# Performance work log

Measured on AMD Instinct MI355X. Metric: run time of the kernel, lower is better.

Reference implementation:

```python
import jax, jax.numpy as jnp
import numpy as np

D = 768
N_HEADS = 12
HEAD_DIM = 64
INNER = N_HEADS * HEAD_DIM
SCALE = HEAD_DIM ** -0.5
EPS = 1e-5


def setup_inputs() -> dict:
    key = jax.random.key(0)
    ks = jax.random.split(key, 7)
    s = 0.02
    return {
        "x": jax.random.normal(ks[0], (2, 2048, D), dtype=jnp.float32),
        "Wq": jax.random.normal(ks[1], (D, INNER), dtype=jnp.float32) * s,
        "Wk": jax.random.normal(ks[2], (D, INNER), dtype=jnp.float32) * s,
        "Wv": jax.random.normal(ks[3], (D, INNER), dtype=jnp.float32) * s,
        "Wo": jax.random.normal(ks[4], (INNER, D), dtype=jnp.float32) * s,
        "bo": jnp.zeros((D,), dtype=jnp.float32),
        "gamma": jnp.ones((D,), dtype=jnp.float32),
        "beta": jnp.zeros((D,), dtype=jnp.float32),
    }


def _layernorm(x, gamma, beta):
    mu = jnp.mean(x, axis=-1, keepdims=True)
    var = jnp.var(x, axis=-1, keepdims=True)
    return (x - mu) * jax.lax.rsqrt(var + EPS) * gamma + beta


def reference(x, Wq, Wk, Wv, Wo, bo, gamma, beta):
    b, n, _ = x.shape
    h = _layernorm(x, gamma, beta)
    # project and split heads: [b, n, inner] -> [b, h, n, d]
    def split(t):
        return t.reshape(b, n, N_HEADS, HEAD_DIM).transpose(0, 2, 1, 3)
    Q = split(h @ Wq)
    K = split(h @ Wk)
    V = split(h @ Wv)
    # NOTE: module applies softmax first, THEN multiplies probs by scale
    attn = jnp.einsum('bhid,bhjd->bhij', Q, K)
    attn = jax.nn.softmax(attn, axis=-1) * SCALE
    vals = jnp.einsum('bhij,bhjd->bhid', attn, V)
    vals = vals.transpose(0, 2, 1, 3).reshape(b, n, INNER)
    out = vals @ Wo + bo
    return x + out
```

## Files before the change

kernel.cpp:

```cpp
#include <hip/hip_runtime.h>
#include <stdint.h>

typedef __bf16 bf16;
typedef __bf16 bf16x8 __attribute__((ext_vector_type(8)));
typedef float  f32x4  __attribute__((ext_vector_type(4)));
typedef unsigned short u16x4 __attribute__((ext_vector_type(4)));
typedef unsigned int   u32x4v __attribute__((ext_vector_type(4)));

#define SEQ   2048
#define DM    768
#define NH    12
#define HD    64
#define ATT_SCALE 0.125f
#define LOG2E 1.44269504f
#define LN_EPS 1e-5f

__device__ __forceinline__ void gload16(const void* g, void* l) {
  __builtin_amdgcn_global_load_lds((const __attribute__((address_space(1))) void*)g,
                                   (__attribute__((address_space(3))) void*)l,
                                   16, 0, 0);
}

__global__ __launch_bounds__(256) void transpose_w(
    const float* __restrict__ Wq, const float* __restrict__ Wk,
    const float* __restrict__ Wv, const float* __restrict__ Wo,
    bf16* __restrict__ Wqkvt, bf16* __restrict__ Wot)
{
  __shared__ float tile[32][33];
  int z = blockIdx.z;
  const float* src = (z==0)?Wq:(z==1)?Wk:(z==2)?Wv:Wo;
  int r0 = blockIdx.y*32, c0 = blockIdx.x*32;
  int tx = threadIdx.x, ty = threadIdx.y;
  #pragma unroll
  for (int i=ty;i<32;i+=8) tile[i][tx] = src[(size_t)(r0+i)*DM + c0+tx];
  __syncthreads();
  bf16* dst = (z<3) ? (Wqkvt + (size_t)z*DM*DM) : Wot;
  #pragma unroll
  for (int i=ty;i<32;i+=8) dst[(size_t)(c0+i)*DM + r0+tx] = (bf16)tile[tx][i];
}

__global__ __launch_bounds__(256) void ln_kernel(
    const float* __restrict__ x, const float* __restrict__ gamma,
    const float* __restrict__ beta, bf16* __restrict__ h)
{
  int row = blockIdx.x;
  const float* xr = x + (size_t)row*DM;
  int t = threadIdx.x;
  float v0 = xr[t], v1 = xr[t+256], v2 = xr[t+512];
  float s = v0+v1+v2;
  float q = v0*v0+v1*v1+v2*v2;
  #pragma unroll
  for (int m=32;m>=1;m>>=1){ s += __shfl_xor(s,m,64); q += __shfl_xor(q,m,64); }
  __shared__ float rs[4], rq[4];
  int w = t>>6;
  if ((t&63)==0){ rs[w]=s; rq[w]=q; }
  __syncthreads();
  float S = rs[0]+rs[1]+rs[2]+rs[3];
  float Q = rq[0]+rq[1]+rq[2]+rq[3];
  float mean = S*(1.0f/DM);
  float var  = Q*(1.0f/DM) - mean*mean;
  float rstd = rsqrtf(var + LN_EPS);
  bf16* hr = h + (size_t)row*DM;
  hr[t]     = (bf16)((v0-mean)*rstd*gamma[t]     + beta[t]);
  hr[t+256] = (bf16)((v1-mean)*rstd*gamma[t+256] + beta[t+256]);
  hr[t+512] = (bf16)((v2-mean)*rstd*gamma[t+512] + beta[t+512]);
}

template<int BM, int BN, int WM, int WN, int EPI>
__global__ __launch_bounds__(256) void gemm_bt(
    const bf16* __restrict__ A, const bf16* __restrict__ Bt, int K,
    bf16* __restrict__ qk, bf16* __restrict__ vt,
    float* __restrict__ out, const float* __restrict__ bo, const float* __restrict__ xres)
{
  constexpr int MF = BM/(WM*16);
  constexpr int NF = BN/(WN*16);
  __shared__ bf16 As[BM][64];
  __shared__ bf16 Bs[BN][64];
  int tid = threadIdx.x, w = tid>>6, la = tid&63;
  int bn = blockIdx.x, bm = blockIdx.y;
  int wm = w / WN, wn = w % WN;
  int g = la>>4, li = la&15;
  int lr = la>>3, lc = (la&7)*8;
  f32x4 acc[MF][NF] = {};

  for (int kt=0; kt<K/64; ++kt) {
    int k0 = kt*64;
    #pragma unroll
    for (int i=0;i<BM/32;i++){ int c=i*4+w;
      gload16(A + ((size_t)(bm*BM + c*8 + lr))*K + k0 + lc, &As[c*8][0]); }
    #pragma unroll
    for (int i=0;i<BN/32;i++){ int c=i*4+w;
      gload16(Bt + ((size_t)(bn*BN + c*8 + lr))*K + k0 + lc, &Bs[c*8][0]); }
    __syncthreads();
    #pragma unroll
    for (int kk=0;kk<2;kk++){
      bf16x8 af[MF], bfr[NF];
      #pragma unroll
      for (int i=0;i<MF;i++) af[i]  = *(const bf16x8*)&As[wm*(BM/WM)+i*16+li][kk*32+g*8];
      #pragma unroll
      for (int j=0;j<NF;j++) bfr[j] = *(const bf16x8*)&Bs[wn*(BN/WN)+j*16+li][kk*32+g*8];
      #pragma unroll
      for (int i=0;i<MF;i++)
        #pragma unroll
        for (int j=0;j<NF;j++)
          acc[i][j] = __builtin_amdgcn_mfma_f32_16x16x32_bf16(af[i], bfr[j], acc[i][j], 0,0,0);
    }
    __syncthreads();
  }

  #pragma unroll
  for (int i=0;i<MF;i++){
    int row0 = bm*BM + wm*(BM/WM) + i*16 + g*4;
    #pragma unroll
    for (int j=0;j<NF;j++){
      int col = bn*BN + wn*(BN/WN) + j*16 + li;
      if (EPI==0){
        if (col < 1536) {
          float qs = (col < 768) ? LOG2E : 1.0f;
          #pragma unroll
          for (int r=0;r<4;r++) qk[(size_t)(row0+r)*1536 + col] = (bf16)(acc[i][j][r]*qs);
        } else {
          int cv = col - 1536; int hh = cv>>6, dd = cv&63;
          int b_ = row0>>11,  n0 = row0&2047;
          u16x4 u;
          #pragma unroll
          for (int r=0;r<4;r++){ bf16 bv = (bf16)acc[i][j][r];
            u[r] = __builtin_bit_cast(unsigned short, bv); }
          *reinterpret_cast<u16x4*>(vt + ((size_t)((b_*NH+hh)*HD+dd))*SEQ + n0) = u;
        }
      } else {
        float bb = bo[col];
        #pragma unroll
        for (int r=0;r<4;r++){ size_t idx = (size_t)(row0+r)*DM + col;
          out[idx] = acc[i][j][r] + bb + xres[idx]; }
      }
    }
  }
}

__global__ __launch_bounds__(256) void attn_kernel(
    const bf16* __restrict__ QK, const bf16* __restrict__ Vt, bf16* __restrict__ vals)
{
  __shared__ bf16 Ks[2][64][64];
  __shared__ bf16 Vs[2][64][64];
  int tid=threadIdx.x, w=tid>>6, la=tid&63;
  int qt=blockIdx.x, hh=blockIdx.y, b=blockIdx.z;
  int g=la>>4, li=la&15;
  int lr=la>>3;
  int lx=li&7;
  int lcs=((la&7)^lr)*8;
  size_t qrow0=(size_t)b*SEQ + qt*64;

  bf16x8 qf[2];
  {
    const bf16* qp = QK + (qrow0 + w*16 + li)*1536 + hh*64;
    qf[0] = *(const bf16x8*)(qp + g*8);
    qf[1] = *(const bf16x8*)(qp + 32 + g*8);
  }

  const bf16* Kbase = QK + (size_t)b*SEQ*1536 + 768 + hh*64;
  const bf16* Vbase = Vt + (size_t)(b*NH+hh)*HD*SEQ;
  #pragma unroll
  for (int i=0;i<2;i++){ int c=i*4+w;
    gload16(Kbase + (size_t)(c*8+lr)*1536 + lcs, &Ks[0][c*8][0]);
    gload16(Vbase + (size_t)(c*8+lr)*SEQ  + lcs, &Vs[0][c*8][0]); }
  __syncthreads();

  f32x4 o[4] = {};
  float lp[4] = {0.f,0.f,0.f,0.f};

  for (int t=0;t<32;t++){
    int buf=t&1;
    if (t) __syncthreads();
    if (t+1<32){
      int j0=(t+1)*64;
      #pragma unroll
      for (int i=0;i<2;i++){ int c=i*4+w;
        gload16(Kbase + (size_t)(j0+c*8+lr)*1536 + lcs, &Ks[buf^1][c*8][0]);
        gload16(Vbase + (size_t)(c*8+lr)*SEQ + j0 + lcs, &Vs[buf^1][c*8][0]); }
    }
    f32x4 s[4] = {};
    #pragma unroll
    for (int kk=0;kk<2;kk++){
      bf16x8 kf[4];
      #pragma unroll
      for (int nf=0;nf<4;nf++){
        int row = nf*16+li;
        kf[nf] = *(const bf16x8*)((const char*)&Ks[buf][0][0] + row*128 + (((kk*4+g)^lx)<<4));
      }
      __builtin_amdgcn_s_setprio(1);
      #pragma unroll
      for (int nf=0;nf<4;nf++)
        s[nf] = __builtin_amdgcn_mfma_f32_16x16x32_bf16(kf[nf], qf[kk], s[nf], 0,0,0);
      __builtin_amdgcn_s_setprio(0);
    }
    float p[4][4];
    #pragma unroll
    for (int nf=0;nf<4;nf++){
      #pragma unroll
      for (int r=0;r<4;r++){
        p[nf][r] = __builtin_amdgcn_exp2f(s[nf][r]);
        lp[nf] += p[nf][r];
      }
    }
    bf16x8 pa[2];
    #pragma unroll
    for (int ks=0;ks<2;ks++){
      unsigned int c00,c01,c10,c11;
      asm("v_cvt_pk_bf16_f32 %0, %1, %2" : "=v"(c00) : "v"(p[2*ks  ][0]), "v"(p[2*ks  ][1]));
      asm("v_cvt_pk_bf16_f32 %0, %1, %2" : "=v"(c01) : "v"(p[2*ks  ][2]), "v"(p[2*ks  ][3]));
      asm("v_cvt_pk_bf16_f32 %0, %1, %2" : "=v"(c10) : "v"(p[2*ks+1][0]), "v"(p[2*ks+1][1]));
      asm("v_cvt_pk_bf16_f32 %0, %1, %2" : "=v"(c11) : "v"(p[2*ks+1][2]), "v"(p[2*ks+1][3]));
      asm("v_permlane32_swap_b32 %0, %1" : "+v"(c00), "+v"(c10));
      asm("v_permlane32_swap_b32 %0, %1" : "+v"(c01), "+v"(c11));
      asm("v_permlane16_swap_b32 %0, %1" : "+v"(c00), "+v"(c10));
      asm("v_permlane16_swap_b32 %0, %1" : "+v"(c01), "+v"(c11));
      u32x4v cc = {c00, c01, c10, c11};
      pa[ks] = __builtin_bit_cast(bf16x8, cc);
    }
    #pragma unroll
    for (int ks=0;ks<2;ks++){
      bf16x8 vb[4];
      #pragma unroll
      for (int df=0;df<4;df++){
        int row = df*16+li;
        vb[df] = *(const bf16x8*)((const char*)&Vs[buf][0][0] + row*128 + (((ks*4+g)^lx)<<4));
      }
      __builtin_amdgcn_s_setprio(1);
      #pragma unroll
      for (int df=0;df<4;df++)
        o[df] = __builtin_amdgcn_mfma_f32_16x16x32_bf16(vb[df], pa[ks], o[df], 0,0,0);
      __builtin_amdgcn_s_setprio(0);
    }
  }
  float lsum = lp[0]+lp[1]+lp[2]+lp[3];
  lsum += __shfl_xor(lsum, 16, 64);
  lsum += __shfl_xor(lsum, 32, 64);
  float fac = ATT_SCALE / lsum;
  bf16* vrow = vals + (qrow0 + w*16 + li)*DM + hh*64;
  #pragma unroll
  for (int df=0;df<4;df++){
    u16x4 u;
    #pragma unroll
    for (int r=0;r<4;r++){
      bf16 bv = (bf16)(o[df][r] * fac);
      u[r] = __builtin_bit_cast(unsigned short, bv);
    }
    *reinterpret_cast<u16x4*>(vrow + df*16 + g*4) = u;
  }
}

extern "C" void kernel_launch(void* const* d_in, const int* in_sizes, int n_in,
                              void* d_out, int out_size, void* d_ws, size_t ws_size,
                              hipStream_t stream)
{
  const float* x     = (const float*)d_in[0];
  const float* Wq    = (const float*)d_in[1];
  const float* Wk    = (const float*)d_in[2];
  const float* Wv    = (const float*)d_in[3];
  const float* Wo    = (const float*)d_in[4];
  const float* bo    = (const float*)d_in[5];
  const float* gamma = (const float*)d_in[6];
  const float* beta  = (const float*)d_in[7];
  float* out = (float*)d_out;
  char* ws = (char*)d_ws;

  bf16* h     = (bf16*)(ws + 0);
  bf16* vals  = (bf16*)(ws + 0);
  bf16* Wqkvt = (bf16*)(ws + 6291456);
  bf16* Wot   = (bf16*)(ws + 9830400);
  bf16* QKb   = (bf16*)(ws + 11010048);
  bf16* Vt    = (bf16*)(ws + 23592960);
  (void)ws_size; (void)in_sizes; (void)n_in; (void)out_size;

  transpose_w<<<dim3(24,24,4), dim3(32,8), 0, stream>>>(Wq,Wk,Wv,Wo, Wqkvt, Wot);
  ln_kernel<<<dim3(4096), dim3(256), 0, stream>>>(x, gamma, beta, h);
  gemm_bt<128,128,2,2,0><<<dim3(18,32), dim3(256), 0, stream>>>(
      h, Wqkvt, DM, QKb, Vt, nullptr, nullptr, nullptr);
  attn_kernel<<<dim3(32,12,2), dim3(256), 0, stream>>>(QKb, Vt, vals);
  gemm_bt<64,64,2,2,1><<<dim3(12,64), dim3(256), 0, stream>>>(
      vals, Wot, DM, nullptr, nullptr, out, bo, x);
}
```

Before: 117.8 us.

## Fuse prep kernels, triple-buffer GEMM and attention loads, remap attention blocks to XCDs

Merges the LayerNorm and weight-transpose kernels into a single launch, removing one launch and its tail. Both GEMMs switch to a 3-stage LDS pipeline with K-step 32, using explicit vmcnt waits and a single barrier per iteration in place of two syncthreads. The attention kernel likewise uses 3-stage K/V buffering and a 1D grid remapped so each XCD handles whole batch-head groups, for better L2 locality of K/V. This costs more LDS per block, which may lower occupancy, and relies on hand-written wait counts being correct.

```diff
diff --git a/kernel.cpp b/kernel.cpp
--- a/kernel.cpp
+++ b/kernel.cpp
@@ -21,49 +21,49 @@
                                    16, 0, 0);
 }
 
-__global__ __launch_bounds__(256) void transpose_w(
+__global__ __launch_bounds__(256) void prep_kernel(
+    const float* __restrict__ x, const float* __restrict__ gamma,
+    const float* __restrict__ beta, bf16* __restrict__ h,
     const float* __restrict__ Wq, const float* __restrict__ Wk,
     const float* __restrict__ Wv, const float* __restrict__ Wo,
     bf16* __restrict__ Wqkvt, bf16* __restrict__ Wot)
 {
-  __shared__ float tile[32][33];
-  int z = blockIdx.z;
-  const float* src = (z==0)?Wq:(z==1)?Wk:(z==2)?Wv:Wo;
-  int r0 = blockIdx.y*32, c0 = blockIdx.x*32;
-  int tx = threadIdx.x, ty = threadIdx.y;
-  #pragma unroll
-  for (int i=ty;i<32;i+=8) tile[i][tx] = src[(size_t)(r0+i)*DM + c0+tx];
-  __syncthreads();
-  bf16* dst = (z<3) ? (Wqkvt + (size_t)z*DM*DM) : Wot;
-  #pragma unroll
-  for (int i=ty;i<32;i+=8) dst[(size_t)(c0+i)*DM + r0+tx] = (bf16)tile[tx][i];
-}
-
-__global__ __launch_bounds__(256) void ln_kernel(
-    const float* __restrict__ x, const float* __restrict__ gamma,
-    const float* __restrict__ beta, bf16* __restrict__ h)
-{
-  int row = blockIdx.x;
-  const float* xr = x + (size_t)row*DM;
-  int t = threadIdx.x;
-  float v0 = xr[t], v1 = xr[t+256], v2 = xr[t+512];
-  float s = v0+v1+v2;
-  float q = v0*v0+v1*v1+v2*v2;
-  #pragma unroll
-  for (int m=32;m>=1;m>>=1){ s += __shfl_xor(s,m,64); q += __shfl_xor(q,m,64); }
-  __shared__ float rs[4], rq[4];
-  int w = t>>6;
-  if ((t&63)==0){ rs[w]=s; rq[w]=q; }
-  __syncthreads();
-  float S = rs[0]+rs[1]+rs[2]+rs[3];
-  float Q = rq[0]+rq[1]+rq[2]+rq[3];
-  float mean = S*(1.0f/DM);
-  float var  = Q*(1.0f/DM) - mean*mean;
-  float rstd = rsqrtf(var + LN_EPS);
-  bf16* hr = h + (size_t)row*DM;
-  hr[t]     = (bf16)((v0-mean)*rstd*gamma[t]     + beta[t]);
-  hr[t+256] = (bf16)((v1-mean)*rstd*gamma[t+256] + beta[t+256]);
-  hr[t+512] = (bf16)((v2-mean)*rstd*gamma[t+512] + beta[t+512]);
+  __shared__ float smem[32*33];
+  int bid = blockIdx.x, t = threadIdx.x;
+  if (bid < 4096) {
+    const float* xr = x + (size_t)bid*DM;
+    float v0 = xr[t], v1 = xr[t+256], v2 = xr[t+512];
+    float s = v0+v1+v2;
+    float q = v0*v0+v1*v1+v2*v2;
+    #pragma unroll
+    for (int m=32;m>=1;m>>=1){ s += __shfl_xor(s,m,64); q += __shfl_xor(q,m,64); }
+    float* rs = smem; float* rq = smem+8;
+    int w = t>>6;
+    if ((t&63)==0){ rs[w]=s; rq[w]=q; }
+    __syncthreads();
+    float S = rs[0]+rs[1]+rs[2]+rs[3];
+    float Q = rq[0]+rq[1]+rq[2]+rq[3];
+    float mean = S*(1.0f/DM);
+    float var  = Q*(1.0f/DM) - mean*mean;
+    float rstd = rsqrtf(var + LN_EPS);
+    bf16* hr = h + (size_t)bid*DM;
+    hr[t]     = (bf16)((v0-mean)*rstd*gamma[t]     + beta[t]);
+    hr[t+256] = (bf16)((v1-mean)*rstd*gamma[t+256] + beta[t+256]);
+    hr[t+512] = (bf16)((v2-mean)*rstd*gamma[t+512] + beta[t+512]);
+  } else {
+    int tb = bid - 4096;
+    int z = tb/576, rem = tb%576;
+    int r0 = (rem/24)*32, c0 = (rem%24)*32;
+    int tx = t&31, ty = t>>5;
+    float (*tile)[33] = (float(*)[33])smem;
+    const float* src = (z==0)?Wq:(z==1)?Wk:(z==2)?Wv:Wo;
+    #pragma unroll
+    for (int i=ty;i<32;i+=8) tile[i][tx] = src[(size_t)(r0+i)*DM + c0+tx];
+    __syncthreads();
+    bf16* dst = (z<3) ? (Wqkvt + (size_t)z*DM*DM) : Wot;
+    #pragma unroll
+    for (int i=ty;i<32;i+=8) dst[(size_t)(c0+i)*DM + r0+tx] = (bf16)tile[tx][i];
+  }
 }
 
 template<int BM, int BN, int WM, int WN, int EPI>
@@ -74,38 +74,53 @@
 {
   constexpr int MF = BM/(WM*16);
   constexpr int NF = BN/(WN*16);
-  __shared__ bf16 As[BM][64];
-  __shared__ bf16 Bs[BN][64];
+  constexpr int GL = BM/64 + BN/64;
+  __shared__ bf16 As[3][BM][32];
+  __shared__ bf16 Bs[3][BN][32];
   int tid = threadIdx.x, w = tid>>6, la = tid&63;
   int bn = blockIdx.x, bm = blockIdx.y;
   int wm = w / WN, wn = w % WN;
   int g = la>>4, li = la&15;
-  int lr = la>>3, lc = (la&7)*8;
+  int sr = la>>2, sc = (la&3)*8;
   f32x4 acc[MF][NF] = {};
-
-  for (int kt=0; kt<K/64; ++kt) {
-    int k0 = kt*64;
-    #pragma unroll
-    for (int i=0;i<BM/32;i++){ int c=i*4+w;
-      gload16(A + ((size_t)(bm*BM + c*8 + lr))*K + k0 + lc, &As[c*8][0]); }
-    #pragma unroll
-    for (int i=0;i<BN/32;i++){ int c=i*4+w;
-      gload16(Bt + ((size_t)(bn*BN + c*8 + lr))*K + k0 + lc, &Bs[c*8][0]); }
-    __syncthreads();
-    #pragma unroll
-    for (int kk=0;kk<2;kk++){
-      bf16x8 af[MF], bfr[NF];
-      #pragma unroll
-      for (int i=0;i<MF;i++) af[i]  = *(const bf16x8*)&As[wm*(BM/WM)+i*16+li][kk*32+g*8];
-      #pragma unroll
-      for (int j=0;j<NF;j++) bfr[j] = *(const bf16x8*)&Bs[wn*(BN/WN)+j*16+li][kk*32+g*8];
-      #pragma unroll
-      for (int i=0;i<MF;i++)
-        #pragma unroll
-        for (int j=0;j<NF;j++)
-          acc[i][j] = __builtin_amdgcn_mfma_f32_16x16x32_bf16(af[i], bfr[j], acc[i][j], 0,0,0);
-    }
-    __syncthreads();
+  const int KT = K/32;
+
+  auto stage = [&](int kt, int bb) {
+    int k0 = kt*32;
+    #pragma unroll
+    for (int i=0;i<BM/64;i++){ int r0 = i*64 + w*16;
+      gload16(A + ((size_t)(bm*BM + r0 + sr))*K + k0 + sc, &As[bb][r0][0]); }
+    #pragma unroll
+    for (int i=0;i<BN/64;i++){ int r0 = i*64 + w*16;
+      gload16(Bt + ((size_t)(bn*BN + r0 + sr))*K + k0 + sc, &Bs[bb][r0][0]); }
+  };
+
+  stage(0,0); stage(1,1);
+  asm volatile("s_waitcnt vmcnt(%0)" :: "n"(GL) : "memory");
+  __builtin_amdgcn_s_barrier();
+  __builtin_amdgcn_sched_barrier(0);
+
+  for (int kt=0; kt<KT; ++kt) {
+    int bb = kt%3;
+    if (kt+2 < KT) stage(kt+2, (kt+2)%3);
+    bf16x8 af[MF], bfr[NF];
+    #pragma unroll
+    for (int i=0;i<MF;i++) af[i]  = *(const bf16x8*)&As[bb][wm*(BM/WM)+i*16+li][g*8];
+    #pragma unroll
+    for (int j=0;j<NF;j++) bfr[j] = *(const bf16x8*)&Bs[bb][wn*(BN/WN)+j*16+li][g*8];
+    __builtin_amdgcn_s_setprio(1);
+    #pragma unroll
+    for (int i=0;i<MF;i++)
+      #pragma unroll
+      for (int j=0;j<NF;j++)
+        acc[i][j] = __builtin_amdgcn_mfma_f32_16x16x32_bf16(af[i], bfr[j], acc[i][j], 0,0,0);
+    __builtin_amdgcn_s_setprio(0);
+    if (kt+1 < KT) {
+      if (kt+2 < KT) asm volatile("s_waitcnt vmcnt(%0)" :: "n"(GL) : "memory");
+      else           asm volatile("s_waitcnt vmcnt(0)" ::: "memory");
+      __builtin_amdgcn_s_barrier();
+      __builtin_amdgcn_sched_barrier(0);
+    }
   }
 
   #pragma unroll
@@ -129,10 +144,10 @@
           *reinterpret_cast<u16x4*>(vt + ((size_t)((b_*NH+hh)*HD+dd))*SEQ + n0) = u;
         }
       } else {
-        float bb = bo[col];
+        float bb2 = bo[col];
         #pragma unroll
         for (int r=0;r<4;r++){ size_t idx = (size_t)(row0+r)*DM + col;
-          out[idx] = acc[i][j][r] + bb + xres[idx]; }
+          out[idx] = acc[i][j][r] + bb2 + xres[idx]; }
       }
     }
   }
@@ -141,10 +156,14 @@
 __global__ __launch_bounds__(256) void attn_kernel(
     const bf16* __restrict__ QK, const bf16* __restrict__ Vt, bf16* __restrict__ vals)
 {
-  __shared__ bf16 Ks[2][64][64];
-  __shared__ bf16 Vs[2][64][64];
+  __shared__ bf16 Ks[3][64][64];
+  __shared__ bf16 Vs[3][64][64];
   int tid=threadIdx.x, w=tid>>6, la=tid&63;
-  int qt=blockIdx.x, hh=blockIdx.y, b=blockIdx.z;
+  int id = blockIdx.x;
+  int xcd = id & 7, idx = id >> 3;
+  int bh  = xcd*3 + (idx>>5);
+  int qt  = idx & 31;
+  int b = bh/NH, hh = bh%NH;
   int g=la>>4, li=la&15;
   int lr=la>>3;
   int lx=li&7;
@@ -160,25 +179,26 @@
 
   const bf16* Kbase = QK + (size_t)b*SEQ*1536 + 768 + hh*64;
   const bf16* Vbase = Vt + (size_t)(b*NH+hh)*HD*SEQ;
-  #pragma unroll
-  for (int i=0;i<2;i++){ int c=i*4+w;
-    gload16(Kbase + (size_t)(c*8+lr)*1536 + lcs, &Ks[0][c*8][0]);
-    gload16(Vbase + (size_t)(c*8+lr)*SEQ  + lcs, &Vs[0][c*8][0]); }
-  __syncthreads();
+
+  auto stage = [&](int tt, int bb) {
+    int j0 = tt*64;
+    #pragma unroll
+    for (int i=0;i<2;i++){ int c=i*4+w;
+      gload16(Kbase + (size_t)(j0 + c*8 + lr)*1536 + lcs, &Ks[bb][c*8][0]);
+      gload16(Vbase + (size_t)(c*8 + lr)*SEQ + j0 + lcs,  &Vs[bb][c*8][0]); }
+  };
+
+  stage(0,0); stage(1,1);
+  asm volatile("s_waitcnt vmcnt(4)" ::: "memory");
+  __builtin_amdgcn_s_barrier();
+  __builtin_amdgcn_sched_barrier(0);
 
   f32x4 o[4] = {};
   float lp[4] = {0.f,0.f,0.f,0.f};
 
   for (int t=0;t<32;t++){
-    int buf=t&1;
-    if (t) __syncthreads();
-    if (t+1<32){
-      int j0=(t+1)*64;
-      #pragma unroll
-      for (int i=0;i<2;i++){ int c=i*4+w;
-        gload16(Kbase + (size_t)(j0+c*8+lr)*1536 + lcs, &Ks[buf^1][c*8][0]);
-        gload16(Vbase + (size_t)(c*8+lr)*SEQ + j0 + lcs, &Vs[buf^1][c*8][0]); }
-    }
+    int bb = t%3;
+    if (t+2 < 32) stage(t+2, (t+2)%3);
     f32x4 s[4] = {};
     #pragma unroll
     for (int kk=0;kk<2;kk++){
@@ -186,7 +206,7 @@
       #pragma unroll
       for (int nf=0;nf<4;nf++){
         int row = nf*16+li;
-        kf[nf] = *(const bf16x8*)((const char*)&Ks[buf][0][0] + row*128 + (((kk*4+g)^lx)<<4));
+        kf[nf] = *(const bf16x8*)((const char*)&Ks[bb][0][0] + row*128 + (((kk*4+g)^lx)<<4));
       }
       __builtin_amdgcn_s_setprio(1);
       #pragma unroll
@@ -224,13 +244,19 @@
       #pragma unroll
       for (int df=0;df<4;df++){
         int row = df*16+li;
-        vb[df] = *(const bf16x8*)((const char*)&Vs[buf][0][0] + row*128 + (((ks*4+g)^lx)<<4));
+        vb[df] = *(const bf16x8*)((const char*)&Vs[bb][0][0] + row*128 + (((ks*4+g)^lx)<<4));
       }
       __builtin_amdgcn_s_setprio(1);
       #pragma unroll
       for (int df=0;df<4;df++)
         o[df] = __builtin_amdgcn_mfma_f32_16x16x32_bf16(vb[df], pa[ks], o[df], 0,0,0);
       __builtin_amdgcn_s_setprio(0);
+    }
+    if (t+1 < 32) {
+      if (t+2 < 32) asm volatile("s_waitcnt vmcnt(4)" ::: "memory");
+      else          asm volatile("s_waitcnt vmcnt(0)" ::: "memory");
+      __builtin_amdgcn_s_barrier();
+      __builtin_amdgcn_sched_barrier(0);
     }
   }
   float lsum = lp[0]+lp[1]+lp[2]+lp[3];
@@ -273,11 +299,11 @@
   bf16* Vt    = (bf16*)(ws + 23592960);
   (void)ws_size; (void)in_sizes; (void)n_in; (void)out_size;
 
-  transpose_w<<<dim3(24,24,4), dim3(32,8), 0, stream>>>(Wq,Wk,Wv,Wo, Wqkvt, Wot);
-  ln_kernel<<<dim3(4096), dim3(256), 0, stream>>>(x, gamma, beta, h);
+  prep_kernel<<<dim3(6400), dim3(256), 0, stream>>>(
+      x, gamma, beta, h, Wq, Wk, Wv, Wo, Wqkvt, Wot);
   gemm_bt<128,128,2,2,0><<<dim3(18,32), dim3(256), 0, stream>>>(
       h, Wqkvt, DM, QKb, Vt, nullptr, nullptr, nullptr);
-  attn_kernel<<<dim3(32,12,2), dim3(256), 0, stream>>>(QKb, Vt, vals);
+  attn_kernel<<<dim3(768), dim3(256), 0, stream>>>(QKb, Vt, vals);
   gemm_bt<64,64,2,2,1><<<dim3(12,64), dim3(256), 0, stream>>>(
       vals, Wot, DM, nullptr, nullptr, out, bo, x);
 }
```

Measured after the change: 103.4 us. 12.2% less time.
